# Kernel optimization log

Hardware: AMD Instinct MI355X
Metric: run time of the kernel (lower is better)

Reference implementation:

```python
import jax, jax.numpy as jnp
import numpy as np

V, E, H, D, A, P = 8000, 384, 512, 512, 512, 128
B, N = 16, 128
NEG = -1.0e9


def _lstm(x, Wih, Whh, b, reverse=False):
    # x: (B, T, E); torch gate order i, f, g, o
    Hd = Whh.shape[1]
    def step(carry, xt):
        h, c = carry
        gates = xt @ Wih.T + h @ Whh.T + b
        i, f, g, o = jnp.split(gates, 4, axis=-1)
        c = jax.nn.sigmoid(f) * c + jax.nn.sigmoid(i) * jnp.tanh(g)
        h = jax.nn.sigmoid(o) * jnp.tanh(c)
        return (h, c), h
    xs = jnp.swapaxes(x, 0, 1)
    if reverse:
        xs = xs[::-1]
    init = (jnp.zeros((x.shape[0], Hd), x.dtype), jnp.zeros((x.shape[0], Hd), x.dtype))
    _, hs = jax.lax.scan(step, init, xs)
    if reverse:
        hs = hs[::-1]
    return jnp.swapaxes(hs, 0, 1)


def _forward(src_ids, src_mask, confusionset_mask, emb, Wih_f, Whh_f, b_f, Wih_b, Whh_b, b_b,
             Wih_d, Whh_d, b_d, W1, W2, v_att, combine_W, combine_b, vocab_W, vocab_b,
             Wg_W, Wg_b, ptr_W, ptr_b, ps_W, ps_b):
    x = emb[src_ids]                                                     # (B,N,E)
    # bidirectional encoder
    enc_hs = jnp.concatenate([_lstm(x, Wih_f, Whh_f, b_f),
                              _lstm(x, Wih_b, Whh_b, b_b, reverse=True)], axis=-1)  # (B,N,2H)
    # decoder LSTMCell unrolled over max_len=N steps (teacher forcing on src chars)
    dec_h = _lstm(x, Wih_d, Whh_d, b_d)                                  # (B,N,D)
    # Bahdanau additive attention
    dterm = dec_h @ W1.T                                                 # (B,N,A)
    eterm = enc_hs @ W2.T                                                # (B,N,A)
    score = jnp.tanh(dterm[:, :, None, :] + eterm[:, None, :, :]) @ v_att  # (B,T,n)
    score = jnp.where(src_mask[:, None, :] == 0, NEG, score)
    alpha = jax.nn.softmax(score, axis=-1)
    context = jnp.einsum('btn,bnh->bth', alpha, enc_hs)                  # (B,T,2H)
    combined = jnp.tanh(jnp.concatenate([dec_h, context], axis=-1) @ combine_W.T + combine_b)  # (B,T,D)
    vocab_logits = combined @ vocab_W.T + vocab_b                        # (B,T,V)
    vocab_logits = jnp.where(confusionset_mask == 0, NEG, vocab_logits)
    # pointer logits: Locj = (t == j) indicator as extra feature
    loc = jnp.eye(N, dtype=combined.dtype)                               # (T,n)
    base = combined @ ptr_W[:, :D].T + ptr_b                             # (B,T,P)
    ph = jnp.tanh(base[:, :, None, :] + loc[None, :, :, None] * ptr_W[:, D][None, None, None, :])  # (B,T,n,P)
    pos_scores = ph @ ps_W + ps_b                                        # (B,T,n)
    sentinel = jnp.tanh(combined @ Wg_W.T + Wg_b).sum(-1, keepdims=True) # (B,T,1)
    pointer_logits = jnp.concatenate([pos_scores, sentinel], axis=-1)    # (B,T,n+1)
    pad_mask = jnp.concatenate([src_mask, jnp.ones((src_mask.shape[0], 1), src_mask.dtype)], axis=1)
    pointer_logits = jnp.where(pad_mask[:, None, :] == 0, NEG, pointer_logits)
    return pointer_logits, vocab_logits


def setup_inputs():
    ks = iter(jax.random.split(jax.random.key(0), 40))
    def g(shape, s=0.05):
        return jax.random.normal(next(ks), shape, jnp.float32) * s
    inp = {
        'src_ids': jax.random.randint(next(ks), (B, N), 1, V),
        'src_mask': jnp.ones((B, N), jnp.int32),
        'confusionset_mask': jax.random.randint(next(ks), (B, N, V), 0, 2).astype(jnp.int32),
        'emb': g((V, E)).at[0].set(0.0),  # padding_idx=0 row zeroed
        'Wih_f': g((4 * H, E)), 'Whh_f': g((4 * H, H)), 'b_f': g((4 * H,)),
        'Wih_b': g((4 * H, E)), 'Whh_b': g((4 * H, H)), 'b_b': g((4 * H,)),
        'Wih_d': g((4 * D, E)), 'Whh_d': g((4 * D, D)), 'b_d': g((4 * D,)),
        'W1': g((A, D)), 'W2': g((A, 2 * H)), 'v_att': g((A,)),
        'combine_W': g((D, D + 2 * H)), 'combine_b': g((D,)),
        'vocab_W': g((V, D)), 'vocab_b': g((V,)),
        'Wg_W': g((D, D)), 'Wg_b': g((D,)),
        'ptr_W': g((P, D + 1)), 'ptr_b': g((P,)),
        'ps_W': g((P,)), 'ps_b': g(()),
    }
    return inp


def reference(src_ids, src_mask, confusionset_mask, emb, Wih_f, Whh_f, b_f, Wih_b, Whh_b, b_b,
              Wih_d, Whh_d, b_d, W1, W2, v_att, combine_W, combine_b, vocab_W, vocab_b,
              Wg_W, Wg_b, ptr_W, ptr_b, ps_W, ps_b):
    return _forward(src_ids, src_mask, confusionset_mask, emb, Wih_f, Whh_f, b_f, Wih_b, Whh_b, b_b,
                    Wih_d, Whh_d, b_d, W1, W2, v_att, combine_W, combine_b, vocab_W, vocab_b,
                    Wg_W, Wg_b, ptr_W, ptr_b, ps_W, ps_b)
```

## Files before the change

kernel.cpp:

```cpp
#include <hip/hip_runtime.h>
#include <hip/hip_bf16.h>
#include <math.h>

#define NEGV -1000000000.0f

static constexpr int B_ = 16, N_ = 128, BN_ = 2048;
static constexpr int E_ = 384, V_ = 8000;

typedef __attribute__((ext_vector_type(8))) short short8v;
typedef __attribute__((ext_vector_type(4))) float f32x4;

__device__ inline float wave_sum(float v) {
#pragma unroll
  for (int o = 32; o; o >>= 1) v += __shfl_xor(v, o);
  return v;
}
__device__ inline float wave_max(float v) {
#pragma unroll
  for (int o = 32; o; o >>= 1) v = fmaxf(v, __shfl_xor(v, o));
  return v;
}
__device__ inline float fast_tanh(float x) {
  return 1.f - 2.f / (1.f + __expf(2.f * x));
}
__device__ inline float fast_sig(float x) {
  return 1.f / (1.f + __expf(-x));
}
__device__ inline int ok16(const f32x4& f) {
  const unsigned a = __builtin_bit_cast(unsigned, f[0]);
  const unsigned b = __builtin_bit_cast(unsigned, f[1]);
  const unsigned c = __builtin_bit_cast(unsigned, f[2]);
  const unsigned d = __builtin_bit_cast(unsigned, f[3]);
  int r = 1;
  r &= ((a & 0xffffu) != 0x7f7fu) & ((a >> 16) != 0x7f7fu);
  r &= ((b & 0xffffu) != 0x7f7fu) & ((b >> 16) != 0x7f7fu);
  r &= ((c & 0xffffu) != 0x7f7fu) & ((c >> 16) != 0x7f7fu);
  r &= ((d & 0xffffu) != 0x7f7fu) & ((d >> 16) != 0x7f7fu);
  return r;
}
__device__ __forceinline__ void gl16(const void* g, void* l) {
  __builtin_amdgcn_global_load_lds((const __attribute__((address_space(1))) void*)g,
                                   (__attribute__((address_space(3))) void*)l, 16, 0, 0);
}

__global__ __launch_bounds__(256) void embed_kernel(
    const int* __restrict__ ids, const float* __restrict__ emb,
    __hip_bfloat16* __restrict__ xb) {
  const int row = blockIdx.x;
  const int id = ids[row];
  for (int e = threadIdx.x; e < E_; e += 256)
    xb[(size_t)row * E_ + e] = __float2bfloat16(emb[(size_t)id * E_ + e]);
}

struct CastArgs {
  const float* s[12];
  unsigned long long d[12];
  int base[12];
  int total;
};
__global__ __launch_bounds__(256) void cast_kernel(CastArgs a) {
  const int nq = a.total >> 2;
  for (int q = blockIdx.x * 256 + threadIdx.x; q < nq; q += gridDim.x * 256) {
    const int e = q << 2;
    int k = 11;
    while (e < a.base[k]) --k;
    const int i = e - a.base[k];
    __hip_bfloat16* dst = (__hip_bfloat16*)a.d[k] + i;
    if (k == 11) {
      const int row = i >> 9, col = i & 511;
      const float* sp = a.s[k] + (size_t)row * 513 + col;
#pragma unroll
      for (int u = 0; u < 4; ++u) dst[u] = __float2bfloat16(sp[u]);
    } else {
      float4 v = *(const float4*)(a.s[k] + i);
      __hip_bfloat16 h0 = __float2bfloat16(v.x), h1 = __float2bfloat16(v.y);
      __hip_bfloat16 h2 = __float2bfloat16(v.z), h3 = __float2bfloat16(v.w);
      ushort4 u4 = {*(unsigned short*)&h0, *(unsigned short*)&h1,
                    *(unsigned short*)&h2, *(unsigned short*)&h3};
      *(ushort4*)dst = u4;
    }
  }
}

template <int ACT, bool MASK>
__global__ __launch_bounds__(256) void bgemm_kernel(
    const __hip_bfloat16* __restrict__ A, int lda,
    const __hip_bfloat16* __restrict__ W, int ldw,
    const float* __restrict__ bias,
    float* __restrict__ C, int ldc,
    __hip_bfloat16* __restrict__ Cb, int ldcb,
    int M, int N, int K,
    const int* __restrict__ mask, int ldm) {
  __shared__ __hip_bfloat16 Al[2][4096];
  __shared__ __hip_bfloat16 Bl[2][4096];
  const int tid = threadIdx.x;
  const int wid = tid >> 6, lane = tid & 63;
  const int m0 = blockIdx.y * 128, n0 = blockIdx.x * 128;
  const int nkt = K >> 5;
  const int rm = (wid >> 1) << 6, rn = (wid & 1) << 6;
  const int lrow = lane & 15, kq = lane >> 4;
  const int fs = ((lrow >> 1) & 3) << 4;

  f32x4 acc[4][4];
#pragma unroll
  for (int i = 0; i < 4; ++i)
#pragma unroll
    for (int j = 0; j < 4; ++j) acc[i][j] = {0.f, 0.f, 0.f, 0.f};

  auto stage = [&](int bi, int kt) {
#pragma unroll
    for (int c = 0; c < 2; ++c) {
      const int p = ((c * 4 + wid) << 6) + lane;
      const int row = p >> 2, cb = (p & 3) << 4;
      const int sw = ((row >> 1) & 3) << 4;
      const unsigned loff = (unsigned)__builtin_amdgcn_readfirstlane((c * 4 + wid) << 10);
      {
        const char* src = (const char*)A + ((size_t)(m0 + row) * lda + (size_t)kt * 32) * 2 + (cb ^ sw);
        gl16(src, (char*)&Al[bi][0] + loff);
      }
      {
        int gr = n0 + row;
        if (gr >= N) gr = N - 1;
        const char* src = (const char*)W + ((size_t)gr * ldw + (size_t)kt * 32) * 2 + (cb ^ sw);
        gl16(src, (char*)&Bl[bi][0] + loff);
      }
    }
  };
  auto compute = [&](int bi) {
    const char* Ab = (const char*)&Al[bi][0];
    const char* Bb = (const char*)&Bl[bi][0];
    const int roff = (kq << 4) ^ fs;
    short8v a[4], b[4];
#pragma unroll
    for (int i = 0; i < 4; ++i)
      a[i] = *(const short8v*)(Ab + (rm + i * 16 + lrow) * 64 + roff);
#pragma unroll
    for (int j = 0; j < 4; ++j)
      b[j] = *(const short8v*)(Bb + (rn + j * 16 + lrow) * 64 + roff);
#pragma unroll
    for (int i = 0; i < 4; ++i)
#pragma unroll
      for (int j = 0; j < 4; ++j)
        acc[i][j] = __builtin_amdgcn_mfma_f32_16x16x32_bf16(a[i], b[j], acc[i][j], 0, 0, 0);
  };

  stage(0, 0);
  for (int kt = 0; kt < nkt; ++kt) {
    __syncthreads();
    if (kt + 1 < nkt) stage((kt + 1) & 1, kt + 1);
    compute(kt & 1);
  }

#pragma unroll
  for (int i = 0; i < 4; ++i) {
#pragma unroll
    for (int r = 0; r < 4; ++r) {
      const int m = m0 + rm + i * 16 + kq * 4 + r;
#pragma unroll
      for (int j = 0; j < 4; ++j) {
        const int n = n0 + rn + j * 16 + lrow;
        if (n < N) {
          float v = acc[i][j][r] + (bias ? bias[n] : 0.f);
          if (ACT == 1) v = tanhf(v);
          if (MASK) {
            if (mask[(size_t)m * ldm + n] == 0) v = NEGV;
          }
          if (C) C[(size_t)m * ldc + n] = v;
          if (Cb) Cb[(size_t)m * ldcb + n] = __float2bfloat16(v);
        }
      }
    }
  }
}

template <int ACT, int TROUT>
__global__ __launch_bounds__(256) void bgemm64_kernel(
    const __hip_bfloat16* __restrict__ A, int lda,
    const __hip_bfloat16* __restrict__ W, int ldw,
    const float* __restrict__ bias, const float* __restrict__ bias2,
    float* __restrict__ C, int ldc, float* __restrict__ C2,
    __hip_bfloat16* __restrict__ Cb, int ldcb,
    int M, int N, int K,
    long aBs, long wBs, long cBs) {
  __shared__ __hip_bfloat16 Al[2][2048];
  __shared__ __hip_bfloat16 Bl[2][2048];
  A += (size_t)blockIdx.z * aBs;
  W += (size_t)blockIdx.z * wBs;
  const int tid = threadIdx.x;
  const int wid = tid >> 6, lane = tid & 63;
  const int m0 = blockIdx.y * 64, n0 = blockIdx.x * 64;
  const int nkt = K >> 5;
  const int rm = (wid >> 1) << 5, rn = (wid & 1) << 5;
  const int lrow = lane & 15, kq = lane >> 4;
  const int fs = ((lrow >> 1) & 3) << 4;

  f32x4 acc[2][2];
#pragma unroll
  for (int i = 0; i < 2; ++i)
#pragma unroll
    for (int j = 0; j < 2; ++j) acc[i][j] = {0.f, 0.f, 0.f, 0.f};

  auto stage = [&](int bi, int kt) {
    const int p = tid;
    const int row = p >> 2, cb = (p & 3) << 4;
    const int sw = ((row >> 1) & 3) << 4;
    const unsigned loff = (unsigned)__builtin_amdgcn_readfirstlane(wid << 10);
    {
      const char* src = (const char*)A + ((size_t)(m0 + row) * lda + (size_t)kt * 32) * 2 + (cb ^ sw);
      gl16(src, (char*)&Al[bi][0] + loff);
    }
    {
      const char* src = (const char*)W + ((size_t)(n0 + row) * ldw + (size_t)kt * 32) * 2 + (cb ^ sw);
      gl16(src, (char*)&Bl[bi][0] + loff);
    }
  };
  auto compute = [&](int bi) {
    const char* Ab = (const char*)&Al[bi][0];
    const char* Bb = (const char*)&Bl[bi][0];
    const int roff = (kq << 4) ^ fs;
    short8v a[2], b[2];
#pragma unroll
    for (int i = 0; i < 2; ++i)
      a[i] = *(const short8v*)(Ab + (rm + i * 16 + lrow) * 64 + roff);
#pragma unroll
    for (int j = 0; j < 2; ++j)
      b[j] = *(const short8v*)(Bb + (rn + j * 16 + lrow) * 64 + roff);
#pragma unroll
    for (int i = 0; i < 2; ++i)
#pragma unroll
      for (int j = 0; j < 2; ++j)
        acc[i][j] = __builtin_amdgcn_mfma_f32_16x16x32_bf16(a[i], b[j], acc[i][j], 0, 0, 0);
  };

  stage(0, 0);
  for (int kt = 0; kt < nkt; ++kt) {
    __syncthreads();
    if (kt + 1 < nkt) stage((kt + 1) & 1, kt + 1);
    compute(kt & 1);
  }

#pragma unroll
  for (int i = 0; i < 2; ++i) {
#pragma unroll
    for (int r = 0; r < 4; ++r) {
      const int m = m0 + rm + i * 16 + kq * 4 + r;
#pragma unroll
      for (int j = 0; j < 2; ++j) {
        const int n = n0 + rn + j * 16 + lrow;
        float v = acc[i][j][r];
        if (TROUT == 2) {
          if (n < 512) {
            C[(size_t)m * ldc + n] = tanhf(v + bias[n]);
          } else {
            C2[(size_t)m * 128 + (n - 512)] = v + bias2[n - 512];
          }
        } else {
          v += (bias ? bias[n] : 0.f);
          if (ACT == 1) v = tanhf(v);
          if (TROUT == 1) {
            Cb[(((size_t)(m >> 7) * 512 + n) << 7) + (m & 127)] = __float2bfloat16(v);
          } else {
            if (C) C[(size_t)m * ldc + n] = v;
            if (Cb) Cb[(size_t)m * ldcb + n + (size_t)blockIdx.z * cBs] = __float2bfloat16(v);
          }
        }
      }
    }
  }
}

__global__ __launch_bounds__(256) void lstm_kernel(
    const __hip_bfloat16* __restrict__ xp16,
    const __hip_bfloat16* __restrict__ whh16,
    __hip_bfloat16* __restrict__ hbuf) {
  const int l = blockIdx.x >> 5, g = blockIdx.x & 31;
  const int tid = threadIdx.x, lane = tid & 63, wid = tid >> 6;
  extern __shared__ char sm[];
  char* smW = sm;
  char* smH = sm + 65536;
  __hip_bfloat16* hout = (__hip_bfloat16*)(sm + 65536 + 16384);

  const __hip_bfloat16* wsrc = whh16 + (size_t)l * 2048 * 512;
  for (int p = tid; p < 4096; p += 256) {
    const int r = p >> 6, cb = (p & 63) << 4;
    const int grow = (r & 3) * 512 + (g << 4) + (r >> 2);
    float4 v = *(const float4*)((const char*)(wsrc + (size_t)grow * 512) + cb);
    *(float4*)(smW + r * 1024 + (cb ^ ((r & 7) << 4))) = v;
  }

  const int lrow = lane & 15, kq = lane >> 4;
  const int swz = (lrow & 7) << 4;
  const char* aB = smW + (wid * 16 + lrow) * 1024;
  const char* bB = smH + lrow * 1024;
  const int dl16 = wid * 4 + kq;
  const int dg = (g << 4) + dl16;
  const int bb = lrow;
  const bool rev = (l == 1);
  const __hip_bfloat16* xl = xp16 + (size_t)l * 2048 * 2048;
  __hip_bfloat16* hb_l = hbuf + (size_t)l * 128 * 8192;
  const int gq = tid >> 3;
  const int b0 = (tid & 7) * 2;
  const int gb = gq * 32;
  const int sw0 = (b0 & 7) << 4, sw1 = ((b0 + 1) & 7) << 4;
  float c = 0.f;

  for (int s = 0; s < 128; ++s) {
    const int t = rev ? 127 - s : s;
    const size_t xro = (size_t)(bb * 128 + t) * 2048 + dg;
    const float xgi = __bfloat162float(xl[xro]);
    const float xgf = __bfloat162float(xl[xro + 512]);
    const float xgg = __bfloat162float(xl[xro + 1024]);
    const float xgo = __bfloat162float(xl[xro + 1536]);

    if (s > 0) {
      if (gq != g) {
        const char* hsrc = (const char*)(hb_l + (size_t)(s - 1) * 8192);
        const unsigned loff = (unsigned)(tid * 64);
        f32x4 q0, q1, q2, q3;
        while (true) {
          asm volatile(
              "global_load_dwordx4 %0, %4, %5 sc0 sc1\n\t"
              "global_load_dwordx4 %1, %4, %5 offset:16 sc0 sc1\n\t"
              "global_load_dwordx4 %2, %4, %5 offset:32 sc0 sc1\n\t"
              "global_load_dwordx4 %3, %4, %5 offset:48 sc0 sc1\n\t"
              "s_waitcnt vmcnt(0)"
              : "=&v"(q0), "=&v"(q1), "=&v"(q2), "=&v"(q3)
              : "v"(loff), "s"(hsrc)
              : "memory");
          if (ok16(q0) & ok16(q1) & ok16(q2) & ok16(q3)) break;
          __builtin_amdgcn_s_sleep(1);
        }
        *(f32x4*)(smH + b0 * 1024 + (gb ^ sw0)) = q0;
        *(f32x4*)(smH + b0 * 1024 + ((gb + 16) ^ sw0)) = q1;
        *(f32x4*)(smH + (b0 + 1) * 1024 + (gb ^ sw1)) = q2;
        *(f32x4*)(smH + (b0 + 1) * 1024 + ((gb + 16) ^ sw1)) = q3;
      }
    } else {
      const f32x4 z = {0.f, 0.f, 0.f, 0.f};
      *(f32x4*)(smH + b0 * 1024 + (gb ^ sw0)) = z;
      *(f32x4*)(smH + b0 * 1024 + ((gb + 16) ^ sw0)) = z;
      *(f32x4*)(smH + (b0 + 1) * 1024 + (gb ^ sw1)) = z;
      *(f32x4*)(smH + (b0 + 1) * 1024 + ((gb + 16) ^ sw1)) = z;
    }
    __syncthreads();

    f32x4 acc0 = {0.f, 0.f, 0.f, 0.f}, acc1 = {0.f, 0.f, 0.f, 0.f};
#pragma unroll
    for (int kt = 0; kt < 16; kt += 2) {
      const int off0 = ((kt * 64 + (kq << 4)) ^ swz);
      const int off1 = (((kt + 1) * 64 + (kq << 4)) ^ swz);
      short8v a0 = *(const short8v*)(aB + off0);
      short8v b0v = *(const short8v*)(bB + off0);
      short8v a1 = *(const short8v*)(aB + off1);
      short8v b1v = *(const short8v*)(bB + off1);
      acc0 = __builtin_amdgcn_mfma_f32_16x16x32_bf16(a0, b0v, acc0, 0, 0, 0);
      acc1 = __builtin_amdgcn_mfma_f32_16x16x32_bf16(a1, b1v, acc1, 0, 0, 0);
    }
    const f32x4 acc = acc0 + acc1;

    const float gi = acc[0] + xgi;
    const float gf = acc[1] + xgf;
    const float gg = acc[2] + xgg;
    const float go = acc[3] + xgo;
    c = fmaf(fast_sig(gf), c, fast_sig(gi) * fast_tanh(gg));
    const float h = fast_sig(go) * fast_tanh(c);
    __hip_bfloat16 hb16 = __float2bfloat16(h);
    const unsigned short hraw = *(unsigned short*)&hb16;
    hout[bb * 16 + dl16] = hb16;
    __syncthreads();
    *(unsigned short*)(smH + bb * 1024 +
                       ((((g << 4) + dl16) * 2) ^ ((bb & 7) << 4))) = hraw;
    if (tid < 32) {
      f32x4 hv4 = *(const f32x4*)((const char*)hout + tid * 16);
      char* hdst = (char*)(hb_l + (size_t)s * 8192);
      asm volatile("global_store_dwordx4 %0, %1, %2 sc0 sc1"
                   :: "v"((unsigned)((g << 9) + tid * 16)), "v"(hv4), "s"(hdst)
                   : "memory");
    }
  }
}

__global__ __launch_bounds__(256) void scatter_kernel(
    const __hip_bfloat16* __restrict__ hbuf,
    __hip_bfloat16* __restrict__ ehsb, __hip_bfloat16* __restrict__ ehsT,
    __hip_bfloat16* __restrict__ catb) {
  const int bid = blockIdx.x;
  const int l = bid >> 7, b = (bid >> 3) & 15, dgrp = bid & 7;
  const int tid = threadIdx.x;
  __shared__ unsigned short tile[64][130];
  const int t4 = tid >> 6, dl = tid & 63;
  const bool rev = (l == 1);
  const char* hb = (const char*)(hbuf + (size_t)l * 128 * 8192);
  const unsigned lineoff = (unsigned)((dgrp * 4 + (dl >> 4)) * 512 + b * 32 + (dl & 15) * 2);
  for (int u = 0; u < 8; ++u) {
    const int tbase = t4 * 4 + u * 16;
    unsigned o[4];
#pragma unroll
    for (int w = 0; w < 4; ++w) {
      const int t = tbase + w;
      const int s = rev ? 127 - t : t;
      o[w] = (unsigned)(s * 16384) + lineoff;
    }
    unsigned h0, h1, h2, h3;
    asm volatile(
        "global_load_ushort %0, %4, %8 sc0 sc1\n\t"
        "global_load_ushort %1, %5, %8 sc0 sc1\n\t"
        "global_load_ushort %2, %6, %8 sc0 sc1\n\t"
        "global_load_ushort %3, %7, %8 sc0 sc1\n\t"
        "s_waitcnt vmcnt(0)"
        : "=&v"(h0), "=&v"(h1), "=&v"(h2), "=&v"(h3)
        : "v"(o[0]), "v"(o[1]), "v"(o[2]), "v"(o[3]), "s"(hb)
        : "memory");
    tile[dl][tbase] = (unsigned short)h0;
    tile[dl][tbase + 1] = (unsigned short)h1;
    tile[dl][tbase + 2] = (unsigned short)h2;
    tile[dl][tbase + 3] = (unsigned short)h3;
  }
  __syncthreads();
  if (l < 2) {
    const int r = tid >> 2, seg = tid & 3;
    ushort4* dstT = (ushort4*)(ehsT + ((size_t)b * 1024 + l * 512 + dgrp * 64 + r) * 128 + seg * 32);
    const unsigned short* srcT = &tile[r][seg * 32];
#pragma unroll
    for (int q = 0; q < 8; ++q) dstT[q] = *(const ushort4*)(srcT + q * 4);
    const int t2 = tid >> 1, half = tid & 1;
    unsigned short buf[32];
#pragma unroll
    for (int q = 0; q < 32; ++q) buf[q] = tile[half * 32 + q][t2];
    ushort4* dstB = (ushort4*)(ehsb + ((size_t)(b * 128 + t2)) * 1024 + l * 512 + dgrp * 64 + half * 32);
#pragma unroll
    for (int q = 0; q < 8; ++q) dstB[q] = *(const ushort4*)(buf + q * 4);
  } else {
    const int t2 = tid >> 1, half = tid & 1;
    unsigned short buf[32];
#pragma unroll
    for (int q = 0; q < 32; ++q) buf[q] = tile[half * 32 + q][t2];
    ushort4* dstB = (ushort4*)(catb + ((size_t)(b * 128 + t2)) * 1536 + dgrp * 64 + half * 32);
#pragma unroll
    for (int q = 0; q < 8; ++q) dstB[q] = *(const ushort4*)(buf + q * 4);
  }
}

__global__ __launch_bounds__(256) void score_kernel(
    const float* __restrict__ dterm, const __hip_bfloat16* __restrict__ etT,
    const float* __restrict__ v_att, const int* __restrict__ src_mask,
    __hip_bfloat16* __restrict__ alphab) {
  const int b = blockIdx.x >> 5, tg = blockIdx.x & 31;
  const int t0 = tg * 4;
  const int tid = threadIdx.x;
  __shared__ float dt[4][512], vs[512], red[4][4][128], al[4][128];
  for (int i = tid; i < 2048; i += 256)
    dt[i >> 9][i & 511] = dterm[((size_t)(b * 128 + t0 + (i >> 9))) * 512 + (i & 511)];
  vs[tid] = v_att[tid];
  vs[tid + 256] = v_att[256 + tid];
  __syncthreads();
  const int n0 = (tid & 63) << 1, ah = tid >> 6;
  {
    const __hip_bfloat16* ep = etT + (((size_t)b * 512 + ah * 128) << 7) + n0;
    const float* vp = vs + ah * 128;
    const float* dp0 = &dt[0][ah * 128];
    const float* dp1 = &dt[1][ah * 128];
    const float* dp2 = &dt[2][ah * 128];
    const float* dp3 = &dt[3][ah * 128];
    float p00 = 0, p01 = 0, p10 = 0, p11 = 0, p20 = 0, p21 = 0, p30 = 0, p31 = 0;
    for (int a = 0; a < 128; ++a) {
      const unsigned u = *(const unsigned*)(ep + ((size_t)a << 7));
      unsigned u0 = u << 16, u1 = u & 0xffff0000u;
      const float e0 = __builtin_bit_cast(float, u0);
      const float e1 = __builtin_bit_cast(float, u1);
      const float va = vp[a];
      p00 = fmaf(va, fast_tanh(dp0[a] + e0), p00);
      p01 = fmaf(va, fast_tanh(dp0[a] + e1), p01);
      p10 = fmaf(va, fast_tanh(dp1[a] + e0), p10);
      p11 = fmaf(va, fast_tanh(dp1[a] + e1), p11);
      p20 = fmaf(va, fast_tanh(dp2[a] + e0), p20);
      p21 = fmaf(va, fast_tanh(dp2[a] + e1), p21);
      p30 = fmaf(va, fast_tanh(dp3[a] + e0), p30);
      p31 = fmaf(va, fast_tanh(dp3[a] + e1), p31);
    }
    red[0][ah][n0] = p00; red[0][ah][n0 + 1] = p01;
    red[1][ah][n0] = p10; red[1][ah][n0 + 1] = p11;
    red[2][ah][n0] = p20; red[2][ah][n0 + 1] = p21;
    red[3][ah][n0] = p30; red[3][ah][n0 + 1] = p31;
  }
  __syncthreads();
#pragma unroll
  for (int tp = 0; tp < 2; ++tp) {
    const int tt = tp * 2 + (tid >> 7);
    const int n = tid & 127;
    float sc = red[tt][0][n] + red[tt][1][n] + red[tt][2][n] + red[tt][3][n];
    if (src_mask[b * 128 + n] == 0) sc = NEGV;
    al[tt][n] = sc;
  }
  __syncthreads();
  {
    const int tt = tid >> 6, lane = tid & 63;
    const float v0 = al[tt][lane], v1 = al[tt][lane + 64];
    const float m = wave_max(fmaxf(v0, v1));
    const float e0 = __expf(v0 - m), e1 = __expf(v1 - m);
    const float inv = 1.f / wave_sum(e0 + e1);
    __hip_bfloat16* ap = alphab + ((size_t)(b * 128 + t0 + tt)) * 128;
    ap[lane] = __float2bfloat16(e0 * inv);
    ap[lane + 64] = __float2bfloat16(e1 * inv);
  }
}

__global__ __launch_bounds__(256) void pointer_kernel(
    const float* __restrict__ base, const float* __restrict__ wgout,
    const float* __restrict__ ptr_W, const float* __restrict__ ps_W,
    const float* __restrict__ ps_b, const int* __restrict__ src_mask,
    float* __restrict__ out0) {
  const int bt = blockIdx.x;
  const int b = bt >> 7, t = bt & 127;
  const int tid = threadIdx.x;
  __shared__ float r0[4], r1[4], r2[4], fin[3];
  float off_p = 0.f, diag_p = 0.f, sent_p;
  if (tid < 128) {
    const float ba = base[(size_t)bt * 128 + tid];
    const float pw = ps_W[tid];
    off_p = tanhf(ba) * pw;
    diag_p = tanhf(ba + ptr_W[tid * 513 + 512]) * pw;
  }
  sent_p = wgout[(size_t)bt * 512 + tid] + wgout[(size_t)bt * 512 + 256 + tid];
  off_p = wave_sum(off_p);
  diag_p = wave_sum(diag_p);
  sent_p = wave_sum(sent_p);
  const int wid = tid >> 6, lane = tid & 63;
  if (lane == 0) { r0[wid] = off_p; r1[wid] = diag_p; r2[wid] = sent_p; }
  __syncthreads();
  if (tid == 0) {
    const float psb = ps_b[0];
    fin[0] = r0[0] + r0[1] + r0[2] + r0[3] + psb;
    fin[1] = r1[0] + r1[1] + r1[2] + r1[3] + psb;
    fin[2] = r2[0] + r2[1] + r2[2] + r2[3];
  }
  __syncthreads();
  const float s_off = fin[0], s_diag = fin[1], sent = fin[2];
  if (tid < 129) {
    float v;
    if (tid == 128) v = sent;
    else {
      v = (tid == t) ? s_diag : s_off;
      if (src_mask[b * 128 + tid] == 0) v = NEGV;
    }
    out0[(size_t)bt * 129 + tid] = v;
  }
}

extern "C" void kernel_launch(void* const* d_in, const int* in_sizes, int n_in,
                              void* d_out, int out_size, void* d_ws, size_t ws_size,
                              hipStream_t stream) {
  const int* src_ids   = (const int*)d_in[0];
  const int* src_mask  = (const int*)d_in[1];
  const int* cmask     = (const int*)d_in[2];
  const float* emb     = (const float*)d_in[3];
  const float* Wih_f   = (const float*)d_in[4];
  const float* Whh_f   = (const float*)d_in[5];
  const float* b_f     = (const float*)d_in[6];
  const float* Wih_b   = (const float*)d_in[7];
  const float* Whh_b   = (const float*)d_in[8];
  const float* b_b     = (const float*)d_in[9];
  const float* Wih_d   = (const float*)d_in[10];
  const float* Whh_d   = (const float*)d_in[11];
  const float* b_d     = (const float*)d_in[12];
  const float* W1      = (const float*)d_in[13];
  const float* W2      = (const float*)d_in[14];
  const float* v_att   = (const float*)d_in[15];
  const float* comb_W  = (const float*)d_in[16];
  const float* comb_b  = (const float*)d_in[17];
  const float* vocab_W = (const float*)d_in[18];
  const float* vocab_b = (const float*)d_in[19];
  const float* Wg_W    = (const float*)d_in[20];
  const float* Wg_b    = (const float*)d_in[21];
  const float* ptr_W   = (const float*)d_in[22];
  const float* ptr_b   = (const float*)d_in[23];
  const float* ps_W    = (const float*)d_in[24];
  const float* ps_b    = (const float*)d_in[25];
  (void)in_sizes; (void)n_in; (void)out_size; (void)ws_size;

  char* wsb = (char*)d_ws;
  size_t o = 0;
  auto alloc = [&](size_t bytes) { char* p = wsb + o; o = (o + bytes + 255) & ~(size_t)255; return p; };
  __hip_bfloat16* xb      = (__hip_bfloat16*)alloc((size_t)BN_ * E_ * 2);
  __hip_bfloat16* xproj16 = (__hip_bfloat16*)alloc((size_t)3 * BN_ * 2048 * 2);
  __hip_bfloat16* ehsb    = (__hip_bfloat16*)alloc((size_t)BN_ * 1024 * 2);
  __hip_bfloat16* ehsT    = (__hip_bfloat16*)alloc((size_t)16 * 1024 * 128 * 2);
  __hip_bfloat16* catb    = (__hip_bfloat16*)alloc((size_t)BN_ * 1536 * 2);
  float* dterm            = (float*)alloc((size_t)BN_ * 512 * 4);
  __hip_bfloat16* etT     = (__hip_bfloat16*)alloc((size_t)16 * 512 * 128 * 2);
  __hip_bfloat16* alphab  = (__hip_bfloat16*)alloc((size_t)BN_ * 128 * 2);
  __hip_bfloat16* combb   = (__hip_bfloat16*)alloc((size_t)BN_ * 512 * 2);
  float* wgout            = (float*)alloc((size_t)BN_ * 512 * 4);
  float* baseb            = (float*)alloc((size_t)BN_ * 128 * 4);
  __hip_bfloat16* hbuf    = (__hip_bfloat16*)alloc((size_t)3 * 128 * 8192 * 2);
  __hip_bfloat16* wihf16  = (__hip_bfloat16*)alloc((size_t)2048 * 384 * 2);
  __hip_bfloat16* wihb16  = (__hip_bfloat16*)alloc((size_t)2048 * 384 * 2);
  __hip_bfloat16* wihd16  = (__hip_bfloat16*)alloc((size_t)2048 * 384 * 2);
  __hip_bfloat16* whh16   = (__hip_bfloat16*)alloc((size_t)3 * 2048 * 512 * 2);
  __hip_bfloat16* w1_16   = (__hip_bfloat16*)alloc((size_t)512 * 512 * 2);
  __hip_bfloat16* w2_16   = (__hip_bfloat16*)alloc((size_t)512 * 1024 * 2);
  __hip_bfloat16* combw16 = (__hip_bfloat16*)alloc((size_t)512 * 1536 * 2);
  __hip_bfloat16* vocw16  = (__hip_bfloat16*)alloc((size_t)8000 * 512 * 2);
  __hip_bfloat16* wgw16   = (__hip_bfloat16*)alloc((size_t)512 * 512 * 2);
  __hip_bfloat16* ptrw16  = (__hip_bfloat16*)alloc((size_t)128 * 512 * 2);

  float* out0 = (float*)d_out;
  float* out1 = out0 + (size_t)BN_ * 129;

  hipError_t e0 = hipMemsetAsync(hbuf, 0x7f, (size_t)3 * 128 * 8192 * 2, stream);
  (void)e0;
  embed_kernel<<<BN_, 256, 0, stream>>>(src_ids, emb, xb);

  CastArgs ca;
  const float* srcs[12] = {Wih_f, Wih_b, Wih_d, Whh_f, Whh_b, Whh_d,
                           W1, W2, comb_W, vocab_W, Wg_W, ptr_W};
  __hip_bfloat16* dsts[12] = {wihf16, wihb16, wihd16, whh16, whh16 + 2048 * 512,
                              whh16 + 2 * 2048 * 512, w1_16, w2_16, combw16,
                              vocw16, wgw16, ptrw16};
  int ns[12] = {2048 * 384, 2048 * 384, 2048 * 384, 2048 * 512, 2048 * 512,
                2048 * 512, 512 * 512, 512 * 1024, 512 * 1536, 8000 * 512,
                512 * 512, 128 * 512};
  int acc = 0;
  for (int k = 0; k < 12; ++k) {
    ca.s[k] = srcs[k];
    ca.d[k] = (unsigned long long)dsts[k];
    ca.base[k] = acc;
    acc += ns[k];
  }
  ca.total = acc;
  cast_kernel<<<2048, 256, 0, stream>>>(ca);

  bgemm_kernel<0, false><<<dim3(16, 16), 256, 0, stream>>>(
      xb, E_, wihf16, E_, b_f, nullptr, 0, xproj16, 2048, BN_, 2048, E_, nullptr, 0);
  bgemm_kernel<0, false><<<dim3(16, 16), 256, 0, stream>>>(
      xb, E_, wihb16, E_, b_b, nullptr, 0, xproj16 + (size_t)BN_ * 2048, 2048, BN_, 2048, E_, nullptr, 0);
  bgemm_kernel<0, false><<<dim3(16, 16), 256, 0, stream>>>(
      xb, E_, wihd16, E_, b_d, nullptr, 0, xproj16 + (size_t)2 * BN_ * 2048, 2048, BN_, 2048, E_, nullptr, 0);

  hipError_t e1 = hipFuncSetAttribute((const void*)lstm_kernel,
                      hipFuncAttributeMaxDynamicSharedMemorySize, 82432);
  (void)e1;
  lstm_kernel<<<96, 256, 82432, stream>>>(xproj16, whh16, hbuf);

  scatter_kernel<<<384, 256, 0, stream>>>(hbuf, ehsb, ehsT, catb);

  bgemm64_kernel<0, 0><<<dim3(8, 32), 256, 0, stream>>>(
      catb, 1536, w1_16, 512, nullptr, nullptr, dterm, 512, nullptr, nullptr, 0,
      BN_, 512, 512, 0, 0, 0);
  bgemm64_kernel<0, 1><<<dim3(8, 32), 256, 0, stream>>>(
      ehsb, 1024, w2_16, 1024, nullptr, nullptr, nullptr, 0, nullptr, etT, 0,
      BN_, 512, 1024, 0, 0, 0);

  score_kernel<<<16 * 32, 256, 0, stream>>>(dterm, etT, v_att, src_mask, alphab);

  bgemm64_kernel<0, 0><<<dim3(16, 2, 16), 256, 0, stream>>>(
      alphab, 128, ehsT, 128, nullptr, nullptr, nullptr, 0, nullptr,
      catb + 512, 1536, 128, 1024, 128, 128 * 128, 1024 * 128, 128 * 1536);

  bgemm64_kernel<1, 0><<<dim3(8, 32), 256, 0, stream>>>(
      catb, 1536, combw16, 1536, comb_b, nullptr, nullptr, 0, nullptr,
      combb, 512, BN_, 512, 1536, 0, 0, 0);

  bgemm_kernel<0, true><<<dim3(63, 16), 256, 0, stream>>>(
      combb, 512, vocw16, 512, vocab_b, out1, V_, nullptr, 0, BN_, V_, 512, cmask, V_);

  bgemm64_kernel<0, 2><<<dim3(10, 32), 256, 0, stream>>>(
      combb, 512, wgw16, 512, Wg_b, ptr_b, wgout, 512, baseb, nullptr, 0,
      BN_, 640, 512, 0, 0, 0);

  pointer_kernel<<<BN_, 256, 0, stream>>>(baseb, wgout, ptr_W, ps_W, ps_b, src_mask, out0);
}
```

Baseline: 657.7 us.

## Fuse LSTM recurrence, scatter and weight casts into one persistent kernel

Merges the LSTM recurrence, the hidden-state scatter/transpose and the remaining weight casts into a single launch. Extra blocks spin-wait on the hbuf sentinel to scatter while the recurrence is still running, and the idle blocks cast the later-stage weights in parallel. The recurrent weights are now cast to bf16 inside the LSTM blocks. Polling is reduced to a single ushort flag per tile before the full load, the block's own h is copied locally, and the global store rotates across waves. It also swaps tanhf for a fast exp-based tanh and pre-scales the attention terms by 2 to drop a multiply in the score loop. Risks include spin-wait deadlock if the scatter blocks occupy CUs before the LSTM blocks are resident, and slightly different tanh precision.

```diff
diff --git a/kernel.cpp b/kernel.cpp
--- a/kernel.cpp
+++ b/kernel.cpp
@@ -23,20 +23,11 @@
 __device__ inline float fast_tanh(float x) {
   return 1.f - 2.f / (1.f + __expf(2.f * x));
 }
+__device__ inline float fast_tanh_pre(float x2) {
+  return 1.f - 2.f / (1.f + __expf(x2));
+}
 __device__ inline float fast_sig(float x) {
   return 1.f / (1.f + __expf(-x));
-}
-__device__ inline int ok16(const f32x4& f) {
-  const unsigned a = __builtin_bit_cast(unsigned, f[0]);
-  const unsigned b = __builtin_bit_cast(unsigned, f[1]);
-  const unsigned c = __builtin_bit_cast(unsigned, f[2]);
-  const unsigned d = __builtin_bit_cast(unsigned, f[3]);
-  int r = 1;
-  r &= ((a & 0xffffu) != 0x7f7fu) & ((a >> 16) != 0x7f7fu);
-  r &= ((b & 0xffffu) != 0x7f7fu) & ((b >> 16) != 0x7f7fu);
-  r &= ((c & 0xffffu) != 0x7f7fu) & ((c >> 16) != 0x7f7fu);
-  r &= ((d & 0xffffu) != 0x7f7fu) & ((d >> 16) != 0x7f7fu);
-  return r;
 }
 __device__ __forceinline__ void gl16(const void* g, void* l) {
   __builtin_amdgcn_global_load_lds((const __attribute__((address_space(1))) void*)g,
@@ -57,16 +48,17 @@
   unsigned long long d[12];
   int base[12];
   int total;
+  int special;
 };
-__global__ __launch_bounds__(256) void cast_kernel(CastArgs a) {
+__device__ inline void cast_body(const CastArgs& a, int gsize, int gid0) {
   const int nq = a.total >> 2;
-  for (int q = blockIdx.x * 256 + threadIdx.x; q < nq; q += gridDim.x * 256) {
+  for (int q = gid0; q < nq; q += gsize) {
     const int e = q << 2;
     int k = 11;
     while (e < a.base[k]) --k;
     const int i = e - a.base[k];
     __hip_bfloat16* dst = (__hip_bfloat16*)a.d[k] + i;
-    if (k == 11) {
+    if (k == a.special) {
       const int row = i >> 9, col = i & 511;
       const float* sp = a.s[k] + (size_t)row * 513 + col;
 #pragma unroll
@@ -80,6 +72,9 @@
       *(ushort4*)dst = u4;
     }
   }
+}
+__global__ __launch_bounds__(256) void cast_kernel(CastArgs a) {
+  cast_body(a, gridDim.x * 256, blockIdx.x * 256 + threadIdx.x);
 }
 
 template <int ACT, bool MASK>
@@ -161,7 +156,7 @@
         const int n = n0 + rn + j * 16 + lrow;
         if (n < N) {
           float v = acc[i][j][r] + (bias ? bias[n] : 0.f);
-          if (ACT == 1) v = tanhf(v);
+          if (ACT == 1) v = fast_tanh(v);
           if (MASK) {
             if (mask[(size_t)m * ldm + n] == 0) v = NEGV;
           }
@@ -250,13 +245,16 @@
         float v = acc[i][j][r];
         if (TROUT == 2) {
           if (n < 512) {
-            C[(size_t)m * ldc + n] = tanhf(v + bias[n]);
+            C[(size_t)m * ldc + n] = fast_tanh(v + bias[n]);
           } else {
             C2[(size_t)m * 128 + (n - 512)] = v + bias2[n - 512];
           }
         } else {
-          v += (bias ? bias[n] : 0.f);
-          if (ACT == 1) v = tanhf(v);
+          if (ACT == 2) v *= 2.f;
+          else {
+            v += (bias ? bias[n] : 0.f);
+            if (ACT == 1) v = fast_tanh(v);
+          }
           if (TROUT == 1) {
             Cb[(((size_t)(m >> 7) * 512 + n) << 7) + (m & 127)] = __float2bfloat16(v);
           } else {
@@ -269,23 +267,107 @@
   }
 }
 
-__global__ __launch_bounds__(256) void lstm_kernel(
+__global__ __launch_bounds__(256) void fused_kernel(
     const __hip_bfloat16* __restrict__ xp16,
-    const __hip_bfloat16* __restrict__ whh16,
-    __hip_bfloat16* __restrict__ hbuf) {
-  const int l = blockIdx.x >> 5, g = blockIdx.x & 31;
-  const int tid = threadIdx.x, lane = tid & 63, wid = tid >> 6;
+    const float* __restrict__ whhF, const float* __restrict__ whhB,
+    const float* __restrict__ whhD,
+    __hip_bfloat16* __restrict__ hbuf,
+    __hip_bfloat16* __restrict__ ehsb, __hip_bfloat16* __restrict__ ehsT,
+    __hip_bfloat16* __restrict__ catb,
+    CastArgs ca2) {
   extern __shared__ char sm[];
+  const int bid = blockIdx.x;
+  const int tid = threadIdx.x;
+
+  if (bid >= 480) {
+    cast_body(ca2, 64 * 256, (bid - 480) * 256 + tid);
+    return;
+  }
+
+  if (bid >= 96) {
+    const int sb = bid - 96;
+    const int l = sb >> 7, b = (sb >> 3) & 15, dgrp = sb & 7;
+    unsigned short (*tile)[130] = (unsigned short(*)[130])sm;
+    const int t4 = tid >> 6, dl = tid & 63;
+    const bool rev = (l == 1);
+    const char* hb = (const char*)(hbuf + (size_t)l * 128 * 8192);
+    const unsigned lineoff = (unsigned)((dgrp * 4 + (dl >> 4)) * 512 + b * 32 + (dl & 15) * 2);
+    for (int u = 0; u < 8; ++u) {
+      const int sbase = t4 * 4 + u * 16;
+      unsigned o0 = (unsigned)(sbase * 16384) + lineoff;
+      unsigned h0, h1, h2, h3;
+      while (true) {
+        asm volatile(
+            "global_load_ushort %0, %4, %8 sc0 sc1\n\t"
+            "global_load_ushort %1, %5, %8 sc0 sc1\n\t"
+            "global_load_ushort %2, %6, %8 sc0 sc1\n\t"
+            "global_load_ushort %3, %7, %8 sc0 sc1\n\t"
+            "s_waitcnt vmcnt(0)"
+            : "=&v"(h0), "=&v"(h1), "=&v"(h2), "=&v"(h3)
+            : "v"(o0), "v"(o0 + 16384u), "v"(o0 + 32768u), "v"(o0 + 49152u),
+              "s"(hb)
+            : "memory");
+        if (((h0 & 0xffffu) != 0x7f7fu) & ((h1 & 0xffffu) != 0x7f7fu) &
+            ((h2 & 0xffffu) != 0x7f7fu) & ((h3 & 0xffffu) != 0x7f7fu)) break;
+        __builtin_amdgcn_s_sleep(8);
+      }
+      const unsigned hv[4] = {h0, h1, h2, h3};
+#pragma unroll
+      for (int w = 0; w < 4; ++w) {
+        const int s = sbase + w;
+        const int t = rev ? 127 - s : s;
+        tile[dl][t] = (unsigned short)hv[w];
+      }
+    }
+    __syncthreads();
+    if (l < 2) {
+      const int r = tid >> 2, seg = tid & 3;
+      ushort4* dstT = (ushort4*)(ehsT + ((size_t)b * 1024 + l * 512 + dgrp * 64 + r) * 128 + seg * 32);
+      const unsigned short* srcT = &tile[r][seg * 32];
+#pragma unroll
+      for (int q = 0; q < 8; ++q) dstT[q] = *(const ushort4*)(srcT + q * 4);
+      const int t2 = tid >> 1, half = tid & 1;
+      unsigned short buf[32];
+#pragma unroll
+      for (int q = 0; q < 32; ++q) buf[q] = tile[half * 32 + q][t2];
+      ushort4* dstB = (ushort4*)(ehsb + ((size_t)(b * 128 + t2)) * 1024 + l * 512 + dgrp * 64 + half * 32);
+#pragma unroll
+      for (int q = 0; q < 8; ++q) dstB[q] = *(const ushort4*)(buf + q * 4);
+    } else {
+      const int t2 = tid >> 1, half = tid & 1;
+      unsigned short buf[32];
+#pragma unroll
+      for (int q = 0; q < 32; ++q) buf[q] = tile[half * 32 + q][t2];
+      ushort4* dstB = (ushort4*)(catb + ((size_t)(b * 128 + t2)) * 1536 + dgrp * 64 + half * 32);
+#pragma unroll
+      for (int q = 0; q < 8; ++q) dstB[q] = *(const ushort4*)(buf + q * 4);
+    }
+    return;
+  }
+
+  const int l = bid >> 5, g = bid & 31;
+  const int lane = tid & 63, wid = tid >> 6;
   char* smW = sm;
   char* smH = sm + 65536;
   __hip_bfloat16* hout = (__hip_bfloat16*)(sm + 65536 + 16384);
 
-  const __hip_bfloat16* wsrc = whh16 + (size_t)l * 2048 * 512;
+  const float* wsrc = (l == 0) ? whhF : ((l == 1) ? whhB : whhD);
+  auto cv = [](float x) -> unsigned {
+    __hip_bfloat16 h = __float2bfloat16(x);
+    return (unsigned)*(unsigned short*)&h;
+  };
   for (int p = tid; p < 4096; p += 256) {
     const int r = p >> 6, cb = (p & 63) << 4;
     const int grow = (r & 3) * 512 + (g << 4) + (r >> 2);
-    float4 v = *(const float4*)((const char*)(wsrc + (size_t)grow * 512) + cb);
-    *(float4*)(smW + r * 1024 + (cb ^ ((r & 7) << 4))) = v;
+    const float* srcp = wsrc + (size_t)grow * 512 + ((p & 63) << 3);
+    float4 u0 = *(const float4*)srcp;
+    float4 u1 = *(const float4*)(srcp + 4);
+    uint4 q;
+    q.x = cv(u0.x) | (cv(u0.y) << 16);
+    q.y = cv(u0.z) | (cv(u0.w) << 16);
+    q.z = cv(u1.x) | (cv(u1.y) << 16);
+    q.w = cv(u1.z) | (cv(u1.w) << 16);
+    *(uint4*)(smW + r * 1024 + (cb ^ ((r & 7) << 4))) = q;
   }
 
   const int lrow = lane & 15, kq = lane >> 4;
@@ -316,24 +398,38 @@
       if (gq != g) {
         const char* hsrc = (const char*)(hb_l + (size_t)(s - 1) * 8192);
         const unsigned loff = (unsigned)(tid * 64);
-        f32x4 q0, q1, q2, q3;
+        unsigned hv;
         while (true) {
           asm volatile(
-              "global_load_dwordx4 %0, %4, %5 sc0 sc1\n\t"
-              "global_load_dwordx4 %1, %4, %5 offset:16 sc0 sc1\n\t"
-              "global_load_dwordx4 %2, %4, %5 offset:32 sc0 sc1\n\t"
-              "global_load_dwordx4 %3, %4, %5 offset:48 sc0 sc1\n\t"
+              "global_load_ushort %0, %1, %2 sc0 sc1\n\t"
               "s_waitcnt vmcnt(0)"
-              : "=&v"(q0), "=&v"(q1), "=&v"(q2), "=&v"(q3)
-              : "v"(loff), "s"(hsrc)
-              : "memory");
-          if (ok16(q0) & ok16(q1) & ok16(q2) & ok16(q3)) break;
+              : "=&v"(hv) : "v"(loff), "s"(hsrc) : "memory");
+          if ((hv & 0xffffu) != 0x7f7fu) break;
           __builtin_amdgcn_s_sleep(1);
         }
+        f32x4 q0, q1, q2, q3;
+        asm volatile(
+            "global_load_dwordx4 %0, %4, %5 sc0 sc1\n\t"
+            "global_load_dwordx4 %1, %4, %5 offset:16 sc0 sc1\n\t"
+            "global_load_dwordx4 %2, %4, %5 offset:32 sc0 sc1\n\t"
+            "global_load_dwordx4 %3, %4, %5 offset:48 sc0 sc1\n\t"
+            "s_waitcnt vmcnt(0)"
+            : "=&v"(q0), "=&v"(q1), "=&v"(q2), "=&v"(q3)
+            : "v"(loff), "s"(hsrc) : "memory");
         *(f32x4*)(smH + b0 * 1024 + (gb ^ sw0)) = q0;
         *(f32x4*)(smH + b0 * 1024 + ((gb + 16) ^ sw0)) = q1;
         *(f32x4*)(smH + (b0 + 1) * 1024 + (gb ^ sw1)) = q2;
         *(f32x4*)(smH + (b0 + 1) * 1024 + ((gb + 16) ^ sw1)) = q3;
+      } else {
+        const char* hl = (const char*)hout + b0 * 32;
+        f32x4 c0 = *(const f32x4*)(hl);
+        f32x4 c1 = *(const f32x4*)(hl + 16);
+        f32x4 c2 = *(const f32x4*)(hl + 32);
+        f32x4 c3 = *(const f32x4*)(hl + 48);
+        *(f32x4*)(smH + b0 * 1024 + (gb ^ sw0)) = c0;
+        *(f32x4*)(smH + b0 * 1024 + ((gb + 16) ^ sw0)) = c1;
+        *(f32x4*)(smH + (b0 + 1) * 1024 + (gb ^ sw1)) = c2;
+        *(f32x4*)(smH + (b0 + 1) * 1024 + ((gb + 16) ^ sw1)) = c3;
       }
     } else {
       const f32x4 z = {0.f, 0.f, 0.f, 0.f};
@@ -365,79 +461,16 @@
     c = fmaf(fast_sig(gf), c, fast_sig(gi) * fast_tanh(gg));
     const float h = fast_sig(go) * fast_tanh(c);
     __hip_bfloat16 hb16 = __float2bfloat16(h);
-    const unsigned short hraw = *(unsigned short*)&hb16;
     hout[bb * 16 + dl16] = hb16;
     __syncthreads();
-    *(unsigned short*)(smH + bb * 1024 +
-                       ((((g << 4) + dl16) * 2) ^ ((bb & 7) << 4))) = hraw;
-    if (tid < 32) {
-      f32x4 hv4 = *(const f32x4*)((const char*)hout + tid * 16);
+
+    if (wid == (s & 3) && (lane < 32)) {
+      f32x4 hv4 = *(const f32x4*)((const char*)hout + lane * 16);
       char* hdst = (char*)(hb_l + (size_t)s * 8192);
       asm volatile("global_store_dwordx4 %0, %1, %2 sc0 sc1"
-                   :: "v"((unsigned)((g << 9) + tid * 16)), "v"(hv4), "s"(hdst)
+                   :: "v"((unsigned)((g << 9) + lane * 16)), "v"(hv4), "s"(hdst)
                    : "memory");
     }
-  }
-}
-
-__global__ __launch_bounds__(256) void scatter_kernel(
-    const __hip_bfloat16* __restrict__ hbuf,
-    __hip_bfloat16* __restrict__ ehsb, __hip_bfloat16* __restrict__ ehsT,
-    __hip_bfloat16* __restrict__ catb) {
-  const int bid = blockIdx.x;
-  const int l = bid >> 7, b = (bid >> 3) & 15, dgrp = bid & 7;
-  const int tid = threadIdx.x;
-  __shared__ unsigned short tile[64][130];
-  const int t4 = tid >> 6, dl = tid & 63;
-  const bool rev = (l == 1);
-  const char* hb = (const char*)(hbuf + (size_t)l * 128 * 8192);
-  const unsigned lineoff = (unsigned)((dgrp * 4 + (dl >> 4)) * 512 + b * 32 + (dl & 15) * 2);
-  for (int u = 0; u < 8; ++u) {
-    const int tbase = t4 * 4 + u * 16;
-    unsigned o[4];
-#pragma unroll
-    for (int w = 0; w < 4; ++w) {
-      const int t = tbase + w;
-      const int s = rev ? 127 - t : t;
-      o[w] = (unsigned)(s * 16384) + lineoff;
-    }
-    unsigned h0, h1, h2, h3;
-    asm volatile(
-        "global_load_ushort %0, %4, %8 sc0 sc1\n\t"
-        "global_load_ushort %1, %5, %8 sc0 sc1\n\t"
-        "global_load_ushort %2, %6, %8 sc0 sc1\n\t"
-        "global_load_ushort %3, %7, %8 sc0 sc1\n\t"
-        "s_waitcnt vmcnt(0)"
-        : "=&v"(h0), "=&v"(h1), "=&v"(h2), "=&v"(h3)
-        : "v"(o[0]), "v"(o[1]), "v"(o[2]), "v"(o[3]), "s"(hb)
-        : "memory");
-    tile[dl][tbase] = (unsigned short)h0;
-    tile[dl][tbase + 1] = (unsigned short)h1;
-    tile[dl][tbase + 2] = (unsigned short)h2;
-    tile[dl][tbase + 3] = (unsigned short)h3;
-  }
-  __syncthreads();
-  if (l < 2) {
-    const int r = tid >> 2, seg = tid & 3;
-    ushort4* dstT = (ushort4*)(ehsT + ((size_t)b * 1024 + l * 512 + dgrp * 64 + r) * 128 + seg * 32);
-    const unsigned short* srcT = &tile[r][seg * 32];
-#pragma unroll
-    for (int q = 0; q < 8; ++q) dstT[q] = *(const ushort4*)(srcT + q * 4);
-    const int t2 = tid >> 1, half = tid & 1;
-    unsigned short buf[32];
-#pragma unroll
-    for (int q = 0; q < 32; ++q) buf[q] = tile[half * 32 + q][t2];
-    ushort4* dstB = (ushort4*)(ehsb + ((size_t)(b * 128 + t2)) * 1024 + l * 512 + dgrp * 64 + half * 32);
-#pragma unroll
-    for (int q = 0; q < 8; ++q) dstB[q] = *(const ushort4*)(buf + q * 4);
-  } else {
-    const int t2 = tid >> 1, half = tid & 1;
-    unsigned short buf[32];
-#pragma unroll
-    for (int q = 0; q < 32; ++q) buf[q] = tile[half * 32 + q][t2];
-    ushort4* dstB = (ushort4*)(catb + ((size_t)(b * 128 + t2)) * 1536 + dgrp * 64 + half * 32);
-#pragma unroll
-    for (int q = 0; q < 8; ++q) dstB[q] = *(const ushort4*)(buf + q * 4);
   }
 }
 
@@ -469,14 +502,14 @@
       const float e0 = __builtin_bit_cast(float, u0);
       const float e1 = __builtin_bit_cast(float, u1);
       const float va = vp[a];
-      p00 = fmaf(va, fast_tanh(dp0[a] + e0), p00);
-      p01 = fmaf(va, fast_tanh(dp0[a] + e1), p01);
-      p10 = fmaf(va, fast_tanh(dp1[a] + e0), p10);
-      p11 = fmaf(va, fast_tanh(dp1[a] + e1), p11);
-      p20 = fmaf(va, fast_tanh(dp2[a] + e0), p20);
-      p21 = fmaf(va, fast_tanh(dp2[a] + e1), p21);
-      p30 = fmaf(va, fast_tanh(dp3[a] + e0), p30);
-      p31 = fmaf(va, fast_tanh(dp3[a] + e1), p31);
+      p00 = fmaf(va, fast_tanh_pre(dp0[a] + e0), p00);
+      p01 = fmaf(va, fast_tanh_pre(dp0[a] + e1), p01);
+      p10 = fmaf(va, fast_tanh_pre(dp1[a] + e0), p10);
+      p11 = fmaf(va, fast_tanh_pre(dp1[a] + e1), p11);
+      p20 = fmaf(va, fast_tanh_pre(dp2[a] + e0), p20);
+      p21 = fmaf(va, fast_tanh_pre(dp2[a] + e1), p21);
+      p30 = fmaf(va, fast_tanh_pre(dp3[a] + e0), p30);
+      p31 = fmaf(va, fast_tanh_pre(dp3[a] + e1), p31);
     }
     red[0][ah][n0] = p00; red[0][ah][n0 + 1] = p01;
     red[1][ah][n0] = p10; red[1][ah][n0 + 1] = p11;
@@ -596,7 +629,6 @@
   __hip_bfloat16* wihf16  = (__hip_bfloat16*)alloc((size_t)2048 * 384 * 2);
   __hip_bfloat16* wihb16  = (__hip_bfloat16*)alloc((size_t)2048 * 384 * 2);
   __hip_bfloat16* wihd16  = (__hip_bfloat16*)alloc((size_t)2048 * 384 * 2);
-  __hip_bfloat16* whh16   = (__hip_bfloat16*)alloc((size_t)3 * 2048 * 512 * 2);
   __hip_bfloat16* w1_16   = (__hip_bfloat16*)alloc((size_t)512 * 512 * 2);
   __hip_bfloat16* w2_16   = (__hip_bfloat16*)alloc((size_t)512 * 1024 * 2);
   __hip_bfloat16* combw16 = (__hip_bfloat16*)alloc((size_t)512 * 1536 * 2);
@@ -611,24 +643,19 @@
   (void)e0;
   embed_kernel<<<BN_, 256, 0, stream>>>(src_ids, emb, xb);
 
-  CastArgs ca;
-  const float* srcs[12] = {Wih_f, Wih_b, Wih_d, Whh_f, Whh_b, Whh_d,
-                           W1, W2, comb_W, vocab_W, Wg_W, ptr_W};
-  __hip_bfloat16* dsts[12] = {wihf16, wihb16, wihd16, whh16, whh16 + 2048 * 512,
-                              whh16 + 2 * 2048 * 512, w1_16, w2_16, combw16,
-                              vocw16, wgw16, ptrw16};
-  int ns[12] = {2048 * 384, 2048 * 384, 2048 * 384, 2048 * 512, 2048 * 512,
-                2048 * 512, 512 * 512, 512 * 1024, 512 * 1536, 8000 * 512,
-                512 * 512, 128 * 512};
-  int acc = 0;
-  for (int k = 0; k < 12; ++k) {
-    ca.s[k] = srcs[k];
-    ca.d[k] = (unsigned long long)dsts[k];
-    ca.base[k] = acc;
-    acc += ns[k];
-  }
-  ca.total = acc;
-  cast_kernel<<<2048, 256, 0, stream>>>(ca);
+  CastArgs c1;
+  {
+    const float* s3[3] = {Wih_f, Wih_b, Wih_d};
+    __hip_bfloat16* d3[3] = {wihf16, wihb16, wihd16};
+    int acc = 0;
+    for (int k = 0; k < 3; ++k) {
+      c1.s[k] = s3[k]; c1.d[k] = (unsigned long long)d3[k]; c1.base[k] = acc;
+      acc += 2048 * 384;
+    }
+    for (int k = 3; k < 12; ++k) { c1.s[k] = nullptr; c1.d[k] = 0; c1.base[k] = 0x7fffffff; }
+    c1.total = acc; c1.special = -1;
+  }
+  cast_kernel<<<1024, 256, 0, stream>>>(c1);
 
   bgemm_kernel<0, false><<<dim3(16, 16), 256, 0, stream>>>(
       xb, E_, wihf16, E_, b_f, nullptr, 0, xproj16, 2048, BN_, 2048, E_, nullptr, 0);
@@ -637,17 +664,30 @@
   bgemm_kernel<0, false><<<dim3(16, 16), 256, 0, stream>>>(
       xb, E_, wihd16, E_, b_d, nullptr, 0, xproj16 + (size_t)2 * BN_ * 2048, 2048, BN_, 2048, E_, nullptr, 0);
 
-  hipError_t e1 = hipFuncSetAttribute((const void*)lstm_kernel,
+  CastArgs c2;
+  {
+    const float* s6[6] = {W1, W2, comb_W, vocab_W, Wg_W, ptr_W};
+    __hip_bfloat16* d6[6] = {w1_16, w2_16, combw16, vocw16, wgw16, ptrw16};
+    int ns[6] = {512 * 512, 512 * 1024, 512 * 1536, 8000 * 512, 512 * 512, 128 * 512};
+    int acc = 0;
+    for (int k = 0; k < 6; ++k) {
+      c2.s[k] = s6[k]; c2.d[k] = (unsigned long long)d6[k]; c2.base[k] = acc;
+      acc += ns[k];
+    }
+    for (int k = 6; k < 12; ++k) { c2.s[k] = nullptr; c2.d[k] = 0; c2.base[k] = 0x7fffffff; }
+    c2.total = acc; c2.special = 5;
+  }
+
+  hipError_t e1 = hipFuncSetAttribute((const void*)fused_kernel,
                       hipFuncAttributeMaxDynamicSharedMemorySize, 82432);
   (void)e1;
-  lstm_kernel<<<96, 256, 82432, stream>>>(xproj16, whh16, hbuf);
-
-  scatter_kernel<<<384, 256, 0, stream>>>(hbuf, ehsb, ehsT, catb);
-
-  bgemm64_kernel<0, 0><<<dim3(8, 32), 256, 0, stream>>>(
+  fused_kernel<<<544, 256, 82432, stream>>>(
+      xproj16, Whh_f, Whh_b, Whh_d, hbuf, ehsb, ehsT, catb, c2);
+
+  bgemm64_kernel<2, 0><<<dim3(8, 32), 256, 0, stream>>>(
       catb, 1536, w1_16, 512, nullptr, nullptr, dterm, 512, nullptr, nullptr, 0,
       BN_, 512, 512, 0, 0, 0);
-  bgemm64_kernel<0, 1><<<dim3(8, 32), 256, 0, stream>>>(
+  bgemm64_kernel<2, 1><<<dim3(8, 32), 256, 0, stream>>>(
       ehsb, 1024, w2_16, 1024, nullptr, nullptr, nullptr, 0, nullptr, etT, 0,
       BN_, 512, 1024, 0, 0, 0);
 
```

Result: slower. 734.1 us (+11.6%).
